# Kernel tuning notes

Hardware: AMD Instinct MI355X
Metric: run time of the kernel (lower is better)

## Reference

```python
import jax, jax.numpy as jnp
import numpy as np

N, E, IN, HID, HEADS, K = 50000, 800000, 7, 64, 4, 4


def _add_self_loops(src, dst, edge_attr, n):
    # PyG add_self_loops with fill_value='mean': loop attr = mean of incoming edge attrs per node
    ones = jnp.ones((src.shape[0],), edge_attr.dtype)
    cnt = jax.ops.segment_sum(ones, dst, num_segments=n)
    loop_attr = jax.ops.segment_sum(edge_attr, dst, num_segments=n) / jnp.maximum(cnt, 1.0)[:, None]
    ar = jnp.arange(n, dtype=src.dtype)
    return (jnp.concatenate([src, ar]), jnp.concatenate([dst, ar]),
            jnp.concatenate([edge_attr, loop_attr], axis=0))


def _gat_conv(x, src, dst, eattr, W, a_src, a_dst, We, a_edge, bias, heads, outc, concat, n):
    xw = (x @ W).reshape(n, heads, outc)                      # [N,H,C]
    al_s = jnp.sum(xw * a_src, -1)                            # [N,H]
    al_d = jnpm if False else jnp.sum(xw * a_dst, -1)         # [N,H]
    ew = (eattr @ We).reshape(-1, heads, outc)                # [E,H,C]
    al_e = jnp.sum(ew * a_edge, -1)                           # [E,H]
    alpha = jax.nn.leaky_relu(al_s[src] + al_d[dst] + al_e, 0.2)
    # segment softmax over incoming edges of each dst node (every node has a self loop)
    m = jax.ops.segment_max(alpha, dst, num_segments=n)
    alpha = jnp.exp(alpha - m[dst])
    denom = jax.ops.segment_sum(alpha, dst, num_segments=n)
    alpha = alpha / (denom[dst] + 1e-16)
    out = jax.ops.segment_sum(xw[src] * alpha[..., None], dst, num_segments=n)  # [N,H,C]
    out = out.reshape(n, heads * outc) if concat else out.mean(axis=1)
    return out + bias


def setup_inputs() -> dict:
    key = jax.random.key(0)
    ks = jax.random.split(key, 24)
    s = lambda d: 1.0 / np.sqrt(d)
    inp = {
        'x': jax.random.uniform(ks[0], (N, IN), jnp.float32),
        'edge_index': jax.random.randint(ks[1], (2, E), 0, N),
        'edge_attr': jax.random.uniform(ks[2], (E, 1), jnp.float32),
        'assignments': jax.random.randint(ks[3], (N,), 0, K),
        # conv1 (heads=4, concat)
        'W1': jax.random.normal(ks[4], (IN, HEADS * HID), jnp.float32) * s(IN),
        'att_src1': jax.random.normal(ks[5], (HEADS, HID), jnp.float32) * s(HID),
        'att_dst1': jax.random.normal(ks[6], (HEADS, HID), jnp.float32) * s(HID),
        'We1': jax.random.normal(ks[7], (1, HEADS * HID), jnp.float32),
        'att_e1': jax.random.normal(ks[8], (HEADS, HID), jnp.float32) * s(HID),
        'b1': jnp.zeros((HEADS * HID,), jnp.float32),
        # conv2 (heads=1, mean)
        'W2': jax.random.normal(ks[9], (HEADS * HID, HID), jnp.float32) * s(HEADS * HID),
        'att_src2': jax.random.normal(ks[10], (1, HID), jnp.float32) * s(HID),
        'att_dst2': jax.random.normal(ks[11], (1, HID), jnp.float32) * s(HID),
        'We2': jax.random.normal(ks[12], (1, HID), jnp.float32),
        'att_e2': jax.random.normal(ks[13], (1, HID), jnp.float32) * s(HID),
        'b2': jnp.zeros((HID,), jnp.float32),
        # actor MLP: Linear(HID+1, HID) -> ReLU -> Linear(HID, 1)
        'A1': jax.random.normal(ks[14], (HID + 1, HID), jnp.float32) * s(HID + 1),
        'c1': jnp.zeros((HID,), jnp.float32),
        'A2': jax.random.normal(ks[15], (HID, 1), jnp.float32) * s(HID),
        'c2': jnp.zeros((1,), jnp.float32),
    }
    return inp


def reference(x, edge_index, edge_attr, assignments,
              W1, att_src1, att_dst1, We1, att_e1, b1,
              W2, att_src2, att_dst2, We2, att_e2, b2,
              A1, c1, A2, c2):
    n = x.shape[0]
    src, dst, ea = _add_self_loops(edge_index[0], edge_index[1], edge_attr, n)
    h = jax.nn.elu(_gat_conv(x, src, dst, ea, W1, att_src1, att_dst1, We1, att_e1, b1,
                             HEADS, HID, True, n))
    h = _gat_conv(h, src, dst, ea, W2, att_src2, att_dst2, We2, att_e2, b2,
                  1, HID, False, n)
    # masked segment-mean pooling over clusters (all K clusters non-empty w.h.p.)
    ones = jnp.ones((n,), h.dtype)
    cnt = jax.ops.segment_sum(ones, assignments, num_segments=K)
    safe = jnp.maximum(cnt, 1.0)
    z = jax.ops.segment_sum(h, assignments, num_segments=K) / safe[:, None]     # [K,HID]
    cf = jax.ops.segment_sum(x[:, 6], assignments, num_segments=K) / safe       # [K]
    nonempty = (cnt > 0)
    z = jnp.where(nonempty[:, None], z, 0.0)
    cf = jnp.where(nonempty, cf, 0.0)
    zcf = jnp.concatenate([z, cf[:, None]], axis=-1)                            # [K,HID+1]
    logits = (jax.nn.relu(zcf @ A1 + c1) @ A2 + c2)[:, 0]                        # [K]
    probs = jax.nn.softmax(logits)[None, :]                                      # [1,K]
    z_flat = z.reshape(1, -1)                                                    # [1,K*HID]
    return probs, z_flat
```

## Files before the change

### kernel.cpp

```cpp
#include <hip/hip_runtime.h>
#include <hip/hip_bf16.h>

#define HEADS 4
#define KCL 4
#define BSHIFT 5
#define BW 32
#define NBUCKMAX 1568
#define BCAP 1024
#define EPT 8
typedef unsigned long long u64;
typedef short short8 __attribute__((ext_vector_type(8)));
typedef float f32x4 __attribute__((ext_vector_type(4)));

__device__ __forceinline__ unsigned short bf16_rne(float f) {
    unsigned int u = __float_as_uint(f);
    u += 0x7FFFu + ((u >> 16) & 1u);
    return (unsigned short)(u >> 16);
}
__device__ __forceinline__ float bf16_to_f32(unsigned short h) {
    return __uint_as_float(((unsigned int)h) << 16);
}


__global__ __launch_bounds__(256) void k_prep_bin(const float* __restrict__ x,
                                                  const float* __restrict__ W1, const float* __restrict__ W2,
                                                  const float* __restrict__ as1, const float* __restrict__ ad1,
                                                  const float* __restrict__ as2, const float* __restrict__ ad2,
                                                  const float* __restrict__ We1, const float* __restrict__ ae1,
                                                  const float* __restrict__ We2, const float* __restrict__ ae2,
                                                  float* __restrict__ ce1, float* __restrict__ ce2,
                                                  float* __restrict__ u_s, float* __restrict__ u_d,
                                                  unsigned short* __restrict__ W2T,
                                                  float* __restrict__ nrec,
                                                  const int* __restrict__ src, const int* __restrict__ dst,
                                                  const float* __restrict__ ea,
                                                  unsigned int* __restrict__ gtail,
                                                  u64* __restrict__ gbuck,
                                                  int N_, int E_, int NB, int nbuck) {
    int t = threadIdx.x;
    if ((int)blockIdx.x >= NB) {
        __shared__ unsigned int cnt[NBUCKMAX];
        __shared__ unsigned int gb[NBUCKMAX];
        for (int i = t; i < nbuck; i += 256) cnt[i] = 0u;
        __syncthreads();
        int bid = blockIdx.x - NB;
        int e0 = bid * (256 * EPT) + t;
        u64 pk[EPT]; int bk[EPT]; unsigned int ls[EPT];
#pragma unroll
        for (int i = 0; i < EPT; i++) {
            int e = e0 + i * 256;
            bool valid = e < E_;
            int s = 0, d = 0; float a = 0.0f;
            if (valid) { s = src[e]; d = dst[e]; a = ea[e]; }
            int b = d >> BSHIFT;
            int lo = d & (BW - 1);
            pk[i] = ((u64)__float_as_uint(a) << 32) | ((u64)(unsigned int)lo << 24) | (unsigned int)s;
            bk[i] = b;
            ls[i] = valid ? atomicAdd(&cnt[b], 1u) : 0u;
        }
        __syncthreads();
        for (int i = t; i < nbuck; i += 256)
            gb[i] = (cnt[i] > 0u) ? atomicAdd(&gtail[i], cnt[i]) : 0u;
        __syncthreads();
#pragma unroll
        for (int i = 0; i < EPT; i++) {
            if (e0 + i * 256 < E_) {
                unsigned int pos = gb[bk[i]] + ls[i];
                if (pos < BCAP) gbuck[(size_t)bk[i] * BCAP + pos] = pk[i];
            }
        }
        return;
    }
    __shared__ float Ps_l[7][4], Pd_l[7][4];
    int h = t >> 6, lane = t & 63;
    for (int i = 0; i < 7; i++) {
        float a = W1[i * 256 + t];
        float ps = a * as1[t];
        float pd = a * ad1[t];
        for (int off = 32; off; off >>= 1) {
            ps += __shfl_down(ps, off, 64);
            pd += __shfl_down(pd, off, 64);
        }
        if (lane == 0) { Ps_l[i][h] = ps; Pd_l[i][h] = pd; }
    }
    if (blockIdx.x == 0) {
        float p = We1[t] * ae1[t];
        for (int off = 32; off; off >>= 1) p += __shfl_down(p, off, 64);
        if (lane == 0) ce1[h] = p;
        if (t < 64) {
            float q = We2[t] * ae2[t];
            for (int off = 32; off; off >>= 1) q += __shfl_down(q, off, 64);
            if (t == 0) ce2[0] = q;
        }
        float us = 0.f, ud = 0.f;
        const float* wr = W2 + t * 64;
        for (int n = 0; n < 64; n++) { us += wr[n] * as2[n]; ud += wr[n] * ad2[n]; }
        u_s[t] = us; u_d[t] = ud;
    }
    int gidx = blockIdx.x * 256 + t;
    if (gidx < 16384) {
        int nn = gidx & 63, k = gidx >> 6;
        W2T[nn * 256 + k] = bf16_rne(W2[k * 64 + nn]);
    }
    __syncthreads();
    int n = gidx;
    if (n >= N_) return;
    float xv[7];
#pragma unroll
    for (int i = 0; i < 7; i++) xv[i] = x[n * 7 + i];
    float4 als = make_float4(0.f, 0.f, 0.f, 0.f);
    float4 ald = make_float4(0.f, 0.f, 0.f, 0.f);
#pragma unroll
    for (int i = 0; i < 7; i++) {
        als.x += xv[i] * Ps_l[i][0]; als.y += xv[i] * Ps_l[i][1];
        als.z += xv[i] * Ps_l[i][2]; als.w += xv[i] * Ps_l[i][3];
        ald.x += xv[i] * Pd_l[i][0]; ald.y += xv[i] * Pd_l[i][1];
        ald.z += xv[i] * Pd_l[i][2]; ald.w += xv[i] * Pd_l[i][3];
    }
    float4* nr = (float4*)(nrec + (size_t)n * 16);
    nr[0] = als;
    nr[1] = ald;
    nr[2] = make_float4(xv[0], xv[1], xv[2], xv[3]);
    nr[3] = make_float4(xv[4], xv[5], xv[6], 0.0f);
}

__global__ __launch_bounds__(256) void k_agg1_xw2g(const unsigned int* __restrict__ gtail,
                                                   const u64* __restrict__ gbuck,
                                                   u64* __restrict__ gpacked,
                                                   int2* __restrict__ idx2,
                                                   const float* __restrict__ nrec,
                                                   const float* __restrict__ ce1,
                                                   const float* __restrict__ W1,
                                                   const float* __restrict__ b1,
                                                   const unsigned short* __restrict__ W2T,
                                                   const float* __restrict__ u_s,
                                                   const float* __restrict__ u_d,
                                                   unsigned short* __restrict__ xw2b,
                                                   float* __restrict__ al_s2,
                                                   float* __restrict__ al_d2, int N_) {
    __shared__ float Xs2[32][36];
    __shared__ __align__(16) unsigned short A_lds[32][264];
    __shared__ u64 esorted[BCAP];
    __shared__ unsigned int rdeg[32], rstart[32], rcur[32];
    __shared__ float als_p[32], ald_p[32];
    int t = threadIdx.x;
    int b = blockIdx.x;
    int m0 = b * 32;
    size_t base = (size_t)b * BCAP;
    u64* raw = (u64*)&A_lds[0][0];
    unsigned int n = gtail[b]; if (n > BCAP) n = BCAP;
    if (t < 32) rdeg[t] = 0u;
    __syncthreads();
    for (unsigned int pos = t; pos < n; pos += 256) {
        u64 p = __builtin_nontemporal_load(&gbuck[base + pos]);
        raw[pos] = p;
        atomicAdd(&rdeg[(unsigned int)(p >> 24) & 31u], 1u);
    }
    __syncthreads();
    if (t < 32) {
        unsigned int deg = rdeg[t];
        unsigned int inc = deg;
#pragma unroll
        for (int off = 1; off < 32; off <<= 1) {
            unsigned int u = __shfl_up(inc, off, 64);
            if (t >= off) inc += u;
        }
        unsigned int start = inc - deg;
        rstart[t] = start; rcur[t] = start;
        if (m0 + t < N_) idx2[m0 + t] = make_int2((int)(base + start), (int)deg);
    }
    __syncthreads();
    for (unsigned int pos = t; pos < n; pos += 256) {
        u64 p = raw[pos];
        unsigned int slot = atomicAdd(&rcur[(unsigned int)(p >> 24) & 31u], 1u);
        esorted[slot] = p;
    }
    __syncthreads();
    for (unsigned int pos = t; pos < n; pos += 256) gpacked[base + pos] = esorted[pos];
    {
        int dl = t >> 3, d = m0 + dl;
        int sub = t & 7, h = sub >> 1, half = sub & 1;
        bool act = d < N_;
        float4 A = make_float4(0.f, 0.f, 0.f, 0.f);
        float4 B = make_float4(0.f, 0.f, 0.f, 0.f);
        if (act) {
            const u64* row = esorted + rstart[dl];
            int cnt = (int)rdeg[dl];
            const float* nd = nrec + (size_t)d * 16;
            float ald = nd[4 + h];
            float ce = ce1[h];
            float easum = 0.0f;
#define E1(J) { \
            u64 p = row[(J)]; \
            int s = (int)(p & 0xFFFFFFu); \
            float a = __uint_as_float((unsigned int)(p >> 32)); \
            const float* ns = nrec + (size_t)s * 16; \
            float als = ns[h]; \
            float4 xa = *(const float4*)(ns + 8); \
            float4 xb = *(const float4*)(ns + 12); \
            easum += a; \
            float v = als + ald + a * ce; \
            v = v > 0.f ? v : 0.2f * v; \
            float w = __expf(v); \
            A.x += w * xa.x; A.y += w * xa.y; A.z += w * xa.z; A.w += w * xa.w; \
            B.x += w * xb.x; B.y += w * xb.y; B.z += w * xb.z; B.w += w; }
            int j = half;
            for (; j + 6 < cnt; j += 8) { E1(j); E1(j + 2); E1(j + 4); E1(j + 6); }
            for (; j < cnt; j += 2) { E1(j); }
#undef E1
            A.x += __shfl_xor(A.x, 1, 64);
            A.y += __shfl_xor(A.y, 1, 64);
            A.z += __shfl_xor(A.z, 1, 64);
            A.w += __shfl_xor(A.w, 1, 64);
            B.x += __shfl_xor(B.x, 1, 64);
            B.y += __shfl_xor(B.y, 1, 64);
            B.z += __shfl_xor(B.z, 1, 64);
            B.w += __shfl_xor(B.w, 1, 64);
            easum += __shfl_xor(easum, 1, 64);
            if (!half) {
                float a_self = easum / fmaxf((float)cnt, 1.0f);
                float v = nd[h] + ald + a_self * ce;
                v = v > 0.f ? v : 0.2f * v;
                float w = __expf(v);
                float4 xa = *(const float4*)(nd + 8);
                float4 xb = *(const float4*)(nd + 12);
                A.x += w * xa.x; A.y += w * xa.y; A.z += w * xa.z; A.w += w * xa.w;
                B.x += w * xb.x; B.y += w * xb.y; B.z += w * xb.z; B.w += w;
            }
        }
        if (!half) {
            *(float4*)&Xs2[dl][h * 8] = A;
            *(float4*)&Xs2[dl][h * 8 + 4] = B;
        }
    }
    __syncthreads();
    {
        int r = t >> 3;
        int kk = t & 7;
        float ps = 0.f, pd = 0.f;
#pragma unroll
        for (int hh = 0; hh < 4; hh++) {
            float xv[7];
#pragma unroll
            for (int i = 0; i < 7; i++) xv[i] = Xs2[r][hh * 8 + i];
            float rw = 1.0f / (Xs2[r][hh * 8 + 7] + 1e-16f);
#pragma unroll
            for (int q = 0; q < 8; q++) {
                int k = hh * 64 + q * 8 + kk;
                float s = 0.f;
#pragma unroll
                for (int i = 0; i < 7; i++) s += xv[i] * W1[i * 256 + k];
                float v = s * rw + b1[k];
                float a = v > 0.f ? v : (__expf(v) - 1.0f);
                ps += a * u_s[k];
                pd += a * u_d[k];
                A_lds[r][k] = bf16_rne(a);
            }
        }
        ps += __shfl_xor(ps, 1, 64); pd += __shfl_xor(pd, 1, 64);
        ps += __shfl_xor(ps, 2, 64); pd += __shfl_xor(pd, 2, 64);
        ps += __shfl_xor(ps, 4, 64); pd += __shfl_xor(pd, 4, 64);
        if (kk == 0) { als_p[r] = ps; ald_p[r] = pd; }
    }
    __syncthreads();
    {
        int w = t >> 6, lane = t & 63;
        int mm = lane & 15, quad = lane >> 4;
        int n0 = w * 16;
        f32x4 acc0 = {0.f, 0.f, 0.f, 0.f};
        f32x4 acc1 = {0.f, 0.f, 0.f, 0.f};
        const unsigned short* bptr = W2T + (size_t)(n0 + mm) * 256;
#pragma unroll
        for (int step = 0; step < 8; step++) {
            int kf = step * 32 + quad * 8;
            short8 bf = *(const short8*)&bptr[kf];
            short8 af0 = *(const short8*)&A_lds[mm][kf];
            short8 af1 = *(const short8*)&A_lds[16 + mm][kf];
            acc0 = __builtin_amdgcn_mfma_f32_16x16x32_bf16(af0, bf, acc0, 0, 0, 0);
            acc1 = __builtin_amdgcn_mfma_f32_16x16x32_bf16(af1, bf, acc1, 0, 0, 0);
        }
#pragma unroll
        for (int r = 0; r < 4; r++) {
            int row0 = m0 + quad * 4 + r;
            if (row0 < N_) xw2b[(size_t)row0 * 64 + n0 + mm] = bf16_rne(acc0[r]);
            int row1 = row0 + 16;
            if (row1 < N_) xw2b[(size_t)row1 * 64 + n0 + mm] = bf16_rne(acc1[r]);
        }
    }
    if (t < 32 && m0 + t < N_) { al_s2[m0 + t] = als_p[t]; al_d2[m0 + t] = ald_p[t]; }
}

__global__ __launch_bounds__(256) void k_agg2p(const int2* __restrict__ idx2,
                                               const u64* __restrict__ gpacked,
                                               const float* __restrict__ al_s2,
                                               const float* __restrict__ al_d2,
                                               const float* __restrict__ ce2,
                                               const unsigned short* __restrict__ xw2b,
                                               const float* __restrict__ x,
                                               const int* __restrict__ assign,
                                               float* __restrict__ zsum, float* __restrict__ cntK,
                                               float* __restrict__ cfK, int N_, int ntiles) {
    __shared__ float lz[256];
    __shared__ float lc[KCL], lf[KCL];
    int t = threadIdx.x;
    lz[t] = 0.0f;
    if (t < KCL) { lc[t] = 0.0f; lf[t] = 0.0f; }
    __syncthreads();
    int dl = t >> 3, sub = t & 7;
    float ce = ce2[0];
    for (int tile = blockIdx.x; tile < ntiles; tile += gridDim.x) {
        int d = tile * 32 + dl;
        if (d >= N_) continue;
        int2 ix = idx2[d];
        const u64* row = gpacked + ix.x;
        int cnt = ix.y;
        float ald = al_d2[d];
        float acc[8];
#pragma unroll
        for (int f = 0; f < 8; f++) acc[f] = 0.0f;
        float wsum = 0.0f, easum = 0.0f;
        const unsigned short* xcol = xw2b + sub * 8;
        int j = 0;
        for (; j + 1 < cnt; j += 2) {
            u64 p0 = row[j], p1 = row[j + 1];
            int s0 = (int)(p0 & 0xFFFFFFu), s1 = (int)(p1 & 0xFFFFFFu);
            float a0 = __uint_as_float((unsigned int)(p0 >> 32));
            float a1 = __uint_as_float((unsigned int)(p1 >> 32));
            float als0 = al_s2[s0], als1 = al_s2[s1];
            short8 g0 = *(const short8*)&xcol[(size_t)s0 * 64];
            short8 g1 = *(const short8*)&xcol[(size_t)s1 * 64];
            easum += a0 + a1;
            float v0 = als0 + ald + a0 * ce; v0 = v0 > 0.f ? v0 : 0.2f * v0;
            float v1 = als1 + ald + a1 * ce; v1 = v1 > 0.f ? v1 : 0.2f * v1;
            float w0 = __expf(v0), w1 = __expf(v1);
            wsum += w0 + w1;
#pragma unroll
            for (int f = 0; f < 8; f++)
                acc[f] += w0 * bf16_to_f32((unsigned short)g0[f])
                        + w1 * bf16_to_f32((unsigned short)g1[f]);
        }
        if (j < cnt) {
            u64 p0 = row[j];
            int s0 = (int)(p0 & 0xFFFFFFu);
            float a0 = __uint_as_float((unsigned int)(p0 >> 32));
            float als0 = al_s2[s0];
            short8 g0 = *(const short8*)&xcol[(size_t)s0 * 64];
            easum += a0;
            float v0 = als0 + ald + a0 * ce; v0 = v0 > 0.f ? v0 : 0.2f * v0;
            float w0 = __expf(v0);
            wsum += w0;
#pragma unroll
            for (int f = 0; f < 8; f++) acc[f] += w0 * bf16_to_f32((unsigned short)g0[f]);
        }
        float a_self = easum / fmaxf((float)cnt, 1.0f);
        float v = al_s2[d] + ald + a_self * ce;
        v = v > 0.f ? v : 0.2f * v;
        float w = __expf(v);
        short8 gd = *(const short8*)&xcol[(size_t)d * 64];
#pragma unroll
        for (int f = 0; f < 8; f++) acc[f] += w * bf16_to_f32((unsigned short)gd[f]);
        wsum += w;
        float rw = 1.0f / (wsum + 1e-16f);
        int a = assign[d];
#pragma unroll
        for (int f = 0; f < 8; f++) atomicAdd(&lz[a * 64 + sub * 8 + f], acc[f] * rw);
        if (sub == 0) {
            atomicAdd(&lc[a], 1.0f);
            atomicAdd(&lf[a], x[d * 7 + 6]);
        }
    }
    __syncthreads();
    atomicAdd(&zsum[t], lz[t]);
    if (t < KCL) {
        atomicAdd(&cntK[t], lc[t]);
        atomicAdd(&cfK[t], lf[t]);
    }
}

__global__ __launch_bounds__(256) void k_head(const float* __restrict__ zsum, const float* __restrict__ cntK,
                                              const float* __restrict__ cfK, const float* __restrict__ b2,
                                              const float* __restrict__ A1, const float* __restrict__ c1,
                                              const float* __restrict__ A2, const float* __restrict__ c2,
                                              float* __restrict__ out) {
    __shared__ float zcf[KCL][65];
    __shared__ float logits[KCL];
    int t = threadIdx.x;
    int k = t >> 6, c = t & 63;
    float cn = cntK[k];
    float z = (cn > 0.f) ? (zsum[k * 64 + c] / fmaxf(cn, 1.0f) + b2[c]) : 0.0f;
    zcf[k][c] = z;
    out[4 + k * 64 + c] = z;
    if (c == 0) zcf[k][64] = (cn > 0.f) ? (cfK[k] / fmaxf(cn, 1.0f)) : 0.0f;
    __syncthreads();
    {
        int j = c;
        float acc = 0.0f;
        for (int i = 0; i < 65; i++) acc += zcf[k][i] * A1[i * 64 + j];
        float hr = fmaxf(acc + c1[j], 0.0f);
        float contrib = hr * A2[j];
        for (int off = 32; off; off >>= 1) contrib += __shfl_down(contrib, off, 64);
        if (j == 0) logits[k] = contrib + c2[0];
    }
    __syncthreads();
    if (t == 0) {
        float m = fmaxf(fmaxf(logits[0], logits[1]), fmaxf(logits[2], logits[3]));
        float e0 = expf(logits[0] - m), e1 = expf(logits[1] - m);
        float e2 = expf(logits[2] - m), e3 = expf(logits[3] - m);
        float s = e0 + e1 + e2 + e3;
        out[0] = e0 / s; out[1] = e1 / s; out[2] = e2 / s; out[3] = e3 / s;
    }
}

extern "C" void kernel_launch(void* const* d_in, const int* in_sizes, int n_in,
                              void* d_out, int out_size, void* d_ws, size_t ws_size,
                              hipStream_t stream) {
    const float* x      = (const float*)d_in[0];
    const int*   ei     = (const int*)d_in[1];
    const float* eattr  = (const float*)d_in[2];
    const int*   assign = (const int*)d_in[3];
    const float* W1     = (const float*)d_in[4];
    const float* as1    = (const float*)d_in[5];
    const float* ad1    = (const float*)d_in[6];
    const float* We1    = (const float*)d_in[7];
    const float* ae1    = (const float*)d_in[8];
    const float* b1     = (const float*)d_in[9];
    const float* W2     = (const float*)d_in[10];
    const float* as2    = (const float*)d_in[11];
    const float* ad2    = (const float*)d_in[12];
    const float* We2    = (const float*)d_in[13];
    const float* ae2    = (const float*)d_in[14];
    const float* b2     = (const float*)d_in[15];
    const float* A1     = (const float*)d_in[16];
    const float* c1     = (const float*)d_in[17];
    const float* A2     = (const float*)d_in[18];
    const float* c2     = (const float*)d_in[19];
    float* out = (float*)d_out;

    const int N_ = in_sizes[0] / 7;
    const int E_ = in_sizes[2];
    const int NB = (N_ + 255) / 256;
    const int nbuck = (N_ + BW - 1) >> BSHIFT;
    const int NBBIN = (E_ + 256 * EPT - 1) / (256 * EPT);
    const int* srcA = ei;
    const int* dstA = ei + E_;

    float* ws = (float*)d_ws;
    size_t Nz = (size_t)N_;
    float* nrec    = ws;
    float* al_s2   = nrec + 16 * Nz;
    float* al_d2   = al_s2 + Nz;
    float* ce1     = al_d2 + Nz;
    float* ce2     = ce1 + 4;
    float* zsum    = ce2 + 4;
    float* cntK    = zsum + 256;
    float* cfK     = cntK + 4;
    unsigned int* gtail  = (unsigned int*)(cfK + 4);
    float* u_s     = (float*)(gtail + NBUCKMAX);
    float* u_d     = u_s + 256;
    unsigned short* xw2b = (unsigned short*)(u_d + 256);
    uintptr_t pp   = (uintptr_t)(xw2b + 64 * Nz);
    u64* gbuck     = (u64*)((pp + 7) & ~(uintptr_t)7);
    u64* gpacked   = gbuck + (size_t)nbuck * BCAP;
    int2* idx2     = (int2*)(gpacked + (size_t)nbuck * BCAP);
    unsigned short* W2T = (unsigned short*)(idx2 + Nz);

    hipMemsetAsync(zsum, 0, (size_t)(264 + NBUCKMAX) * sizeof(float), stream);

    k_prep_bin<<<NB + NBBIN, 256, 0, stream>>>(x, W1, W2, as1, ad1, as2, ad2,
                                               We1, ae1, We2, ae2,
                                               ce1, ce2, u_s, u_d, W2T, nrec,
                                               srcA, dstA, eattr, gtail, gbuck,
                                               N_, E_, NB, nbuck);

    k_agg1_xw2g<<<nbuck, 256, 0, stream>>>(gtail, gbuck, gpacked, idx2, nrec, ce1,
                                           W1, b1, W2T, u_s, u_d,
                                           xw2b, al_s2, al_d2, N_);

    k_agg2p<<<512, 256, 0, stream>>>(idx2, gpacked, al_s2, al_d2, ce2, xw2b,
                                     x, assign, zsum, cntK, cfK, N_, nbuck);

    k_head<<<1, 256, 0, stream>>>(zsum, cntK, cfK, b2, A1, c1, A2, c2, out);
}
```

Baseline: 219.8 us.

## Launch one block per tile in agg2 and shard global reduction atomics across slices

```diff
diff --git a/kernel.cpp b/kernel.cpp
--- a/kernel.cpp
+++ b/kernel.cpp
@@ -8,6 +8,7 @@
 #define NBUCKMAX 1568
 #define BCAP 1024
 #define EPT 8
+#define NSLICE 8
 typedef unsigned long long u64;
 typedef short short8 __attribute__((ext_vector_type(8)));
 typedef float f32x4 __attribute__((ext_vector_type(4)));
@@ -298,8 +299,7 @@
                                                const unsigned short* __restrict__ xw2b,
                                                const float* __restrict__ x,
                                                const int* __restrict__ assign,
-                                               float* __restrict__ zsum, float* __restrict__ cntK,
-                                               float* __restrict__ cfK, int N_, int ntiles) {
+                                               float* __restrict__ zsumS, int N_) {
     __shared__ float lz[256];
     __shared__ float lc[KCL], lf[KCL];
     int t = threadIdx.x;
@@ -308,9 +308,8 @@
     __syncthreads();
     int dl = t >> 3, sub = t & 7;
     float ce = ce2[0];
-    for (int tile = blockIdx.x; tile < ntiles; tile += gridDim.x) {
-        int d = tile * 32 + dl;
-        if (d >= N_) continue;
+    int d = blockIdx.x * 32 + dl;
+    if (d < N_) {
         int2 ix = idx2[d];
         const u64* row = gpacked + ix.x;
         int cnt = ix.y;
@@ -320,38 +319,24 @@
         for (int f = 0; f < 8; f++) acc[f] = 0.0f;
         float wsum = 0.0f, easum = 0.0f;
         const unsigned short* xcol = xw2b + sub * 8;
+#define EDGE2(P) { \
+        int s_ = (int)((P) & 0xFFFFFFu); \
+        float a_ = __uint_as_float((unsigned int)((P) >> 32)); \
+        float als_ = al_s2[s_]; \
+        short8 g_ = *(const short8*)&xcol[(size_t)s_ * 64]; \
+        easum += a_; \
+        float v_ = als_ + ald + a_ * ce; v_ = v_ > 0.f ? v_ : 0.2f * v_; \
+        float w_ = __expf(v_); \
+        wsum += w_; \
+        _Pragma("unroll") \
+        for (int f = 0; f < 8; f++) acc[f] += w_ * bf16_to_f32((unsigned short)g_[f]); }
         int j = 0;
-        for (; j + 1 < cnt; j += 2) {
-            u64 p0 = row[j], p1 = row[j + 1];
-            int s0 = (int)(p0 & 0xFFFFFFu), s1 = (int)(p1 & 0xFFFFFFu);
-            float a0 = __uint_as_float((unsigned int)(p0 >> 32));
-            float a1 = __uint_as_float((unsigned int)(p1 >> 32));
-            float als0 = al_s2[s0], als1 = al_s2[s1];
-            short8 g0 = *(const short8*)&xcol[(size_t)s0 * 64];
-            short8 g1 = *(const short8*)&xcol[(size_t)s1 * 64];
-            easum += a0 + a1;
-            float v0 = als0 + ald + a0 * ce; v0 = v0 > 0.f ? v0 : 0.2f * v0;
-            float v1 = als1 + ald + a1 * ce; v1 = v1 > 0.f ? v1 : 0.2f * v1;
-            float w0 = __expf(v0), w1 = __expf(v1);
-            wsum += w0 + w1;
-#pragma unroll
-            for (int f = 0; f < 8; f++)
-                acc[f] += w0 * bf16_to_f32((unsigned short)g0[f])
-                        + w1 * bf16_to_f32((unsigned short)g1[f]);
-        }
-        if (j < cnt) {
-            u64 p0 = row[j];
-            int s0 = (int)(p0 & 0xFFFFFFu);
-            float a0 = __uint_as_float((unsigned int)(p0 >> 32));
-            float als0 = al_s2[s0];
-            short8 g0 = *(const short8*)&xcol[(size_t)s0 * 64];
-            easum += a0;
-            float v0 = als0 + ald + a0 * ce; v0 = v0 > 0.f ? v0 : 0.2f * v0;
-            float w0 = __expf(v0);
-            wsum += w0;
-#pragma unroll
-            for (int f = 0; f < 8; f++) acc[f] += w0 * bf16_to_f32((unsigned short)g0[f]);
-        }
+        for (; j + 3 < cnt; j += 4) {
+            u64 p0 = row[j], p1 = row[j + 1], p2 = row[j + 2], p3 = row[j + 3];
+            EDGE2(p0); EDGE2(p1); EDGE2(p2); EDGE2(p3);
+        }
+        for (; j < cnt; j++) { u64 p0 = row[j]; EDGE2(p0); }
+#undef EDGE2
         float a_self = easum / fmaxf((float)cnt, 1.0f);
         float v = al_s2[d] + ald + a_self * ce;
         v = v > 0.f ? v : 0.2f * v;
@@ -370,15 +355,15 @@
         }
     }
     __syncthreads();
-    atomicAdd(&zsum[t], lz[t]);
+    float* zs = zsumS + (size_t)(blockIdx.x & (NSLICE - 1)) * 264;
+    atomicAdd(&zs[t], lz[t]);
     if (t < KCL) {
-        atomicAdd(&cntK[t], lc[t]);
-        atomicAdd(&cfK[t], lf[t]);
-    }
-}
-
-__global__ __launch_bounds__(256) void k_head(const float* __restrict__ zsum, const float* __restrict__ cntK,
-                                              const float* __restrict__ cfK, const float* __restrict__ b2,
+        atomicAdd(&zs[256 + t], lc[t]);
+        atomicAdd(&zs[260 + t], lf[t]);
+    }
+}
+
+__global__ __launch_bounds__(256) void k_head(const float* __restrict__ zsumS, const float* __restrict__ b2,
                                               const float* __restrict__ A1, const float* __restrict__ c1,
                                               const float* __restrict__ A2, const float* __restrict__ c2,
                                               float* __restrict__ out) {
@@ -386,11 +371,18 @@
     __shared__ float logits[KCL];
     int t = threadIdx.x;
     int k = t >> 6, c = t & 63;
-    float cn = cntK[k];
-    float z = (cn > 0.f) ? (zsum[k * 64 + c] / fmaxf(cn, 1.0f) + b2[c]) : 0.0f;
+    float zs = 0.0f, cn = 0.0f, cf = 0.0f;
+#pragma unroll
+    for (int s = 0; s < NSLICE; s++) {
+        const float* sl = zsumS + (size_t)s * 264;
+        zs += sl[k * 64 + c];
+        cn += sl[256 + k];
+        cf += sl[260 + k];
+    }
+    float z = (cn > 0.f) ? (zs / fmaxf(cn, 1.0f) + b2[c]) : 0.0f;
     zcf[k][c] = z;
     out[4 + k * 64 + c] = z;
-    if (c == 0) zcf[k][64] = (cn > 0.f) ? (cfK[k] / fmaxf(cn, 1.0f)) : 0.0f;
+    if (c == 0) zcf[k][64] = (cn > 0.f) ? (cf / fmaxf(cn, 1.0f)) : 0.0f;
     __syncthreads();
     {
         int j = c;
@@ -451,10 +443,8 @@
     float* al_d2   = al_s2 + Nz;
     float* ce1     = al_d2 + Nz;
     float* ce2     = ce1 + 4;
-    float* zsum    = ce2 + 4;
-    float* cntK    = zsum + 256;
-    float* cfK     = cntK + 4;
-    unsigned int* gtail  = (unsigned int*)(cfK + 4);
+    float* zsumS   = ce2 + 4;
+    unsigned int* gtail = (unsigned int*)(zsumS + NSLICE * 264);
     float* u_s     = (float*)(gtail + NBUCKMAX);
     float* u_d     = u_s + 256;
     unsigned short* xw2b = (unsigned short*)(u_d + 256);
@@ -464,7 +454,7 @@
     int2* idx2     = (int2*)(gpacked + (size_t)nbuck * BCAP);
     unsigned short* W2T = (unsigned short*)(idx2 + Nz);
 
-    hipMemsetAsync(zsum, 0, (size_t)(264 + NBUCKMAX) * sizeof(float), stream);
+    hipMemsetAsync(zsumS, 0, (size_t)(NSLICE * 264 + NBUCKMAX) * sizeof(float), stream);
 
     k_prep_bin<<<NB + NBBIN, 256, 0, stream>>>(x, W1, W2, as1, ad1, as2, ad2,
                                                We1, ae1, We2, ae2,
@@ -476,8 +466,8 @@
                                            W1, b1, W2T, u_s, u_d,
                                            xw2b, al_s2, al_d2, N_);
 
-    k_agg2p<<<512, 256, 0, stream>>>(idx2, gpacked, al_s2, al_d2, ce2, xw2b,
-                                     x, assign, zsum, cntK, cfK, N_, nbuck);
-
-    k_head<<<1, 256, 0, stream>>>(zsum, cntK, cfK, b2, A1, c1, A2, c2, out);
-}
+    k_agg2p<<<nbuck, 256, 0, stream>>>(idx2, gpacked, al_s2, al_d2, ce2, xw2b,
+                                       x, assign, zsumS, N_);
+
+    k_head<<<1, 256, 0, stream>>>(zsumS, b2, A1, c1, A2, c2, out);
+}
```

New measurement: 205.0 us. -6.7%, faster.
